# Performance work log

Measured on AMD Instinct MI355X. Metric: run time of the kernel, lower is better.

## Reference

```python
import jax, jax.numpy as jnp
import numpy as np
import math


def _conv1x1(x, w, b):
    # x: [B,C,H,W], w: [O,C], b: [O] -> [B,O,H,W]
    return jnp.einsum('oc,bchw->bohw', w, x) + b[None, :, None, None]


def _attn_branch(x, f_w, f_b, g_w, g_b, h_w, h_b, gamma):
    B, C, H, W = x.shape
    N = H * W
    k_dim = C // 8
    f = _conv1x1(x, f_w, f_b).reshape(B, k_dim, N)  # [B,k,N]
    g = _conv1x1(x, g_w, g_b).reshape(B, k_dim, N)  # [B,k,N]
    # attention[b, n, m] = sum_k f[b,k,n] * g[b,k,m] / sqrt(k_dim)
    scores = jnp.einsum('bkn,bkm->bnm', f, g) / math.sqrt(k_dim)
    attn = jax.nn.softmax(scores, axis=2)  # softmax over last dim (dim=2)
    h = _conv1x1(x, h_w, h_b).reshape(B, C, N)  # [B,C,N]
    sa_map = jnp.einsum('bcn,bnm->bcm', h, attn).reshape(B, C, H, W)
    return gamma[0] * sa_map + x


def setup_inputs() -> dict:
    key = jax.random.key(0)
    ks = jax.random.split(key, 8)
    B, C, H, W = 4, 256, 64, 64
    kd = C // 8
    scale_in = 1.0 / math.sqrt(C)
    return {
        'x1': jax.random.normal(ks[0], (B, C, H, W), jnp.float32),
        'x2': jax.random.normal(ks[1], (B, C, H, W), jnp.float32),
        'f_w': jax.random.normal(ks[2], (kd, C), jnp.float32) * scale_in,
        'f_b': jnp.zeros((kd,), jnp.float32),
        'g_w': jax.random.normal(ks[3], (kd, C), jnp.float32) * scale_in,
        'g_b': jnp.zeros((kd,), jnp.float32),
        'h1_w': jax.random.normal(ks[4], (C, C), jnp.float32) * scale_in,
        'h1_b': jnp.zeros((C,), jnp.float32),
        'h2_w': jax.random.normal(ks[5], (C, C), jnp.float32) * scale_in,
        'h2_b': jnp.zeros((C,), jnp.float32),
        'gamma1': jax.random.normal(ks[6], (1,), jnp.float32),
        'gamma2': jax.random.normal(ks[7], (1,), jnp.float32),
    }


def reference(x1, x2, f_w, f_b, g_w, g_b, h1_w, h1_b, h2_w, h2_b, gamma1, gamma2):
    y1 = _attn_branch(x1, f_w, f_b, g_w, g_b, h1_w, h1_b, gamma1)
    y2 = _attn_branch(x2, f_w, f_b, g_w, g_b, h2_w, h2_b, gamma2)
    return (y1, y2)
```

## Files before the change

### kernel.cpp

```cpp
#include <hip/hip_runtime.h>
#include <hip/hip_bf16.h>
#include <math.h>

#define NDIM 4096
#define CDIM 256
#define KD   32
#define SCALE 0.17677669529663687f
#define SHIFT 8.0f

typedef __attribute__((ext_vector_type(8))) short short8;
typedef __attribute__((ext_vector_type(4))) float f32x4;
typedef unsigned short u16;
typedef unsigned int u32;

__device__ __forceinline__ u32 f2bf(float x) {
  union { float f; u32 u; } v; v.f = x;
  return (v.u + 0x7FFFu + ((v.u >> 16) & 1u)) >> 16;
}

__device__ __forceinline__ u32 pack_bf16x2(float a, float b) {
  __hip_bfloat162 h2 = __float22bfloat162_rn(make_float2(a, b));
  u32 r;
  __builtin_memcpy(&r, &h2, 4);
  return r;
}

#define MFMA16(a, b, c) __builtin_amdgcn_mfma_f32_16x16x32_bf16((a), (b), (c), 0, 0, 0)

__global__ void cast_all_kernel(const float* __restrict__ h1w,
                                const float* __restrict__ h2w,
                                const float* __restrict__ fw,
                                const float* __restrict__ gw,
                                u16* __restrict__ dst) {
  int i = blockIdx.x * 256 + threadIdx.x;
  float v;
  if (i < 65536) v = h1w[i];
  else if (i < 131072) v = h2w[i - 65536];
  else if (i < 139264) v = fw[i - 131072];
  else v = gw[i - 139264];
  dst[i] = (u16)f2bf(v);
}

__global__ __launch_bounds__(256) void transpose_cast_kernel(
    const float* __restrict__ x1, const float* __restrict__ x2,
    u16* __restrict__ xt) {
  __shared__ float ts[64][68];
  const int t = threadIdx.x;
  const int ntile = blockIdx.x * 64, Ctile = blockIdx.y * 64, z = blockIdx.z;
  const float* xb = ((z >> 2) ? x2 : x1) + (size_t)(z & 3) * CDIM * NDIM;
  u16* xtb = xt + (size_t)z * NDIM * CDIM;
  const int r = t >> 4, c4 = (t & 15) * 4;
#pragma unroll
  for (int i = 0; i < 4; i++) {
    float4 v = *(const float4*)&xb[(size_t)(Ctile + r + i * 16) * NDIM + ntile + c4];
    *(float4*)&ts[r + i * 16][c4] = v;
  }
  __syncthreads();
  const int n = t >> 2, Cg = (t & 3) * 16;
  u32 pk[8];
#pragma unroll
  for (int j = 0; j < 8; j++) {
    u32 lo = f2bf(ts[Cg + 2 * j][n]);
    u32 hi = f2bf(ts[Cg + 2 * j + 1][n]);
    pk[j] = lo | (hi << 16);
  }
  uint4* dst = (uint4*)&xtb[(size_t)(ntile + n) * CDIM + Ctile + Cg];
  dst[0] = make_uint4(pk[0], pk[1], pk[2], pk[3]);
  dst[1] = make_uint4(pk[4], pk[5], pk[6], pk[7]);
}

__global__ __launch_bounds__(256) void conv_fg_kernel(
    const u16* __restrict__ Wf, const float* __restrict__ fbias,
    const u16* __restrict__ Wg, const float* __restrict__ gbias,
    const u16* __restrict__ xt, u16* __restrict__ ftT, u16* __restrict__ gtT) {
  const int t = threadIdx.x, w = t >> 6, l = t & 63, li = l & 15, q = l >> 4;
  const int ntile = blockIdx.x * 64, bb = blockIdx.y;
  const u16* xtb = xt + (size_t)bb * NDIM * CDIM;
  f32x4 zero4 = {0.f, 0.f, 0.f, 0.f};
  f32x4 acc[2][2];
  for (int i = 0; i < 2; i++) for (int j = 0; j < 2; j++) acc[i][j] = zero4;
  const int nrow = ntile + w * 16 + li;

  for (int k0 = 0; k0 < CDIM; k0 += 32) {
    short8 bx = *(const short8*)&xtb[(size_t)nrow * CDIM + k0 + q * 8];
    short8 af0 = *(const short8*)&Wf[(size_t)(li) * CDIM + k0 + q * 8];
    short8 af1 = *(const short8*)&Wf[(size_t)(16 + li) * CDIM + k0 + q * 8];
    short8 ag0 = *(const short8*)&Wg[(size_t)(li) * CDIM + k0 + q * 8];
    short8 ag1 = *(const short8*)&Wg[(size_t)(16 + li) * CDIM + k0 + q * 8];
    acc[0][0] = MFMA16(af0, bx, acc[0][0]);
    acc[0][1] = MFMA16(af1, bx, acc[0][1]);
    acc[1][0] = MFMA16(ag0, bx, acc[1][0]);
    acc[1][1] = MFMA16(ag1, bx, acc[1][1]);
  }
  u16* outs[2] = {ftT + (size_t)bb * NDIM * KD, gtT + (size_t)bb * NDIM * KD};
  const float* biases[2] = {fbias, gbias};
#pragma unroll
  for (int fg = 0; fg < 2; fg++) {
#pragma unroll
    for (int os = 0; os < 2; os++) {
      float b0 = biases[fg][os * 16 + q * 4 + 0];
      float b1 = biases[fg][os * 16 + q * 4 + 1];
      float b2 = biases[fg][os * 16 + q * 4 + 2];
      float b3 = biases[fg][os * 16 + q * 4 + 3];
      u32 p0 = f2bf(acc[fg][os][0] + b0) | (f2bf(acc[fg][os][1] + b1) << 16);
      u32 p1 = f2bf(acc[fg][os][2] + b2) | (f2bf(acc[fg][os][3] + b3) << 16);
      *(uint2*)&outs[fg][(size_t)nrow * KD + os * 16 + q * 4] = make_uint2(p0, p1);
    }
  }
}

__global__ __launch_bounds__(256) void stats_kernel(
    const u16* __restrict__ ft, const u16* __restrict__ gt,
    float* __restrict__ L) {
  __shared__ float zred[32][64];
  const int t = threadIdx.x, w = t >> 6, l = t & 63, li = l & 15, q = l >> 4;
  const int n0 = blockIdx.x * 32;
  const int bb = blockIdx.z * 4 + blockIdx.y;
  const u16* ftb = ft + (size_t)bb * NDIM * KD;
  const u16* gtb = gt + (size_t)bb * NDIM * KD;
  f32x4 zero4 = {0.f, 0.f, 0.f, 0.f};

  short8 a0 = *(const short8*)&ftb[(size_t)(n0 + li) * KD + q * 8];
  short8 a1 = *(const short8*)&ftb[(size_t)(n0 + 16 + li) * KD + q * 8];
  f32x4 z0 = zero4, z1 = zero4;

#pragma unroll 2
  for (int it = 0; it < 64; it++) {
    int m = (it * 4 + w) * 16;
    short8 bf = *(const short8*)&gtb[(size_t)(m + li) * KD + q * 8];
    f32x4 S0 = MFMA16(a0, bf, zero4);
    f32x4 S1 = MFMA16(a1, bf, zero4);
#pragma unroll
    for (int reg = 0; reg < 4; reg++) {
      z0[reg] += __expf(S0[reg] * SCALE - SHIFT);
      z1[reg] += __expf(S1[reg] * SCALE - SHIFT);
    }
  }
#pragma unroll
  for (int reg = 0; reg < 4; reg++) {
    zred[q * 4 + reg][w * 16 + li] = z0[reg];
    zred[16 + q * 4 + reg][w * 16 + li] = z1[reg];
  }
  __syncthreads();
  const int r = t >> 3, i8 = t & 7;
  float4 s1 = *(const float4*)&zred[r][i8 * 8];
  float4 s2 = *(const float4*)&zred[r][i8 * 8 + 4];
  float sum = s1.x + s1.y + s1.z + s1.w + s2.x + s2.y + s2.z + s2.w;
  sum += __shfl_xor(sum, 1, 8);
  sum += __shfl_xor(sum, 2, 8);
  sum += __shfl_xor(sum, 4, 8);
  if (i8 == 0) L[(size_t)bb * NDIM + n0 + r] = SHIFT + __logf(sum);
}

__global__ __launch_bounds__(256) void conv_h_kernel(
    const u16* __restrict__ Wall, const float* __restrict__ b1,
    const float* __restrict__ b2, const u16* __restrict__ xt,
    const float* __restrict__ L, u16* __restrict__ outH) {
  const int t = threadIdx.x, w = t >> 6, l = t & 63, li = l & 15, q = l >> 4;
  const int ntile = blockIdx.x * 64;
  const int o0 = blockIdx.y * 64 + w * 16;
  const int bb = blockIdx.z, branch = bb >> 2;
  const u16* W = Wall + (size_t)branch * CDIM * CDIM;
  const float* bias = branch ? b2 : b1;
  const u16* xtb = xt + (size_t)bb * NDIM * CDIM;
  const float* Lb = L + (size_t)bb * NDIM;
  u16* ob = outH + (size_t)bb * CDIM * NDIM;
  f32x4 zero4 = {0.f, 0.f, 0.f, 0.f};
  f32x4 acc[4];
  for (int i = 0; i < 4; i++) acc[i] = zero4;

  for (int k0 = 0; k0 < CDIM; k0 += 32) {
    short8 a = *(const short8*)&W[(size_t)(o0 + li) * CDIM + k0 + q * 8];
#pragma unroll
    for (int ns = 0; ns < 4; ns++) {
      short8 bf = *(const short8*)&xtb[(size_t)(ntile + ns * 16 + li) * CDIM + k0 + q * 8];
      acc[ns] = MFMA16(a, bf, acc[ns]);
    }
  }
  float bv[4];
#pragma unroll
  for (int reg = 0; reg < 4; reg++) bv[reg] = bias[o0 + q * 4 + reg];
#pragma unroll
  for (int ns = 0; ns < 4; ns++) {
    int n = ntile + ns * 16 + li;
    float ex = __expf(-Lb[n]);
#pragma unroll
    for (int reg = 0; reg < 4; reg++) {
      int c = o0 + q * 4 + reg;
      ob[(size_t)c * NDIM + n] = (u16)f2bf((acc[ns][reg] + bv[reg]) * ex);
    }
  }
}

__global__ __launch_bounds__(1024, 4) void apply_kernel(
    const u16* __restrict__ ft, const u16* __restrict__ gt,
    const u16* __restrict__ h,
    const float* __restrict__ x1, const float* __restrict__ x2,
    const float* __restrict__ gamma1, const float* __restrict__ gamma2,
    float* __restrict__ out) {
  __shared__ u16 Pt[2][128][132];
  const int t = threadIdx.x, w = t >> 6, l = t & 63, li = l & 15, q = l >> 4;
  const int bid = blockIdx.x;
  const int bb = bid & 7;
  const int mtile = (bid >> 3) * 128;
  const int br = bb >> 2, b = bb & 3;
  const u16* ftb = ft + (size_t)bb * NDIM * KD;
  const u16* gtb = gt + (size_t)bb * NDIM * KD;
  const u16* hb = h + (size_t)bb * CDIM * NDIM;
  const float* xb = (br ? x2 : x1) + (size_t)b * CDIM * NDIM;
  const float gmv = br ? gamma2[0] : gamma1[0];
  float* ob = out + (size_t)bb * CDIM * NDIM;

  const bool producer = (w & 1) == 0;
  const int pidx = w >> 1;
  const int c0 = (w >> 1) * 32;
  f32x4 zero4 = {0.f, 0.f, 0.f, 0.f};

  short8 gfrag;
  if (producer)
    gfrag = *(const short8*)&gtb[(size_t)(mtile + pidx * 16 + li) * KD + q * 8];

  f32x4 acc[8][2];
#pragma unroll
  for (int i = 0; i < 8; i++)
#pragma unroll
    for (int j = 0; j < 2; j++) acc[i][j] = zero4;

  for (int i = 0; i <= 32; i++) {
    if (producer) {
      if (i < 32) {
        const int n0 = i * 128, buf = i & 1;
        short8 af[8];
#pragma unroll
        for (int j = 0; j < 8; j++)
          af[j] = *(const short8*)&ftb[(size_t)(n0 + j * 16 + li) * KD + q * 8];
#pragma unroll
        for (int j = 0; j < 8; j++) {
          f32x4 S = MFMA16(af[j], gfrag, zero4);
          u32 p0 = pack_bf16x2(__expf(S[0] * SCALE), __expf(S[1] * SCALE));
          u32 p1 = pack_bf16x2(__expf(S[2] * SCALE), __expf(S[3] * SCALE));
          *(uint2*)&Pt[buf][pidx * 16 + li][j * 16 + q * 4] = make_uint2(p0, p1);
        }
      }
    } else {
      if (i >= 1) {
        const int n0 = (i - 1) * 128, buf = (i - 1) & 1;
        short8 ah[2][2];
#pragma unroll
        for (int cs = 0; cs < 2; cs++)
          ah[0][cs] = *(const short8*)
              &hb[(size_t)(c0 + cs * 16 + li) * NDIM + n0 + q * 8];
        __builtin_amdgcn_s_setprio(1);
#pragma unroll
        for (int kh = 0; kh < 4; kh++) {
          if (kh < 3) {
#pragma unroll
            for (int cs = 0; cs < 2; cs++)
              ah[(kh + 1) & 1][cs] = *(const short8*)
                  &hb[(size_t)(c0 + cs * 16 + li) * NDIM + n0 + (kh + 1) * 32 + q * 8];
          }
#pragma unroll
          for (int ms = 0; ms < 8; ms++) {
            short8 bm = *(const short8*)&Pt[buf][ms * 16 + li][kh * 32 + q * 8];
            acc[ms][0] = MFMA16(bm, ah[kh & 1][0], acc[ms][0]);
            acc[ms][1] = MFMA16(bm, ah[kh & 1][1], acc[ms][1]);
          }
        }
        __builtin_amdgcn_s_setprio(0);
      }
    }
    asm volatile("s_waitcnt lgkmcnt(0)" ::: "memory");
    __builtin_amdgcn_s_barrier();
  }

  if (!producer) {
#pragma unroll
    for (int ms = 0; ms < 8; ms++) {
#pragma unroll
      for (int cs = 0; cs < 2; cs++) {
        int c = c0 + cs * 16 + li;
        int m = mtile + ms * 16 + q * 4;
        size_t idx = (size_t)c * NDIM + m;
        float4 xv = *(const float4*)&xb[idx];
        float4 o;
        o.x = gmv * acc[ms][cs][0] + xv.x;
        o.y = gmv * acc[ms][cs][1] + xv.y;
        o.z = gmv * acc[ms][cs][2] + xv.z;
        o.w = gmv * acc[ms][cs][3] + xv.w;
        *(float4*)&ob[idx] = o;
      }
    }
  }
}

extern "C" void kernel_launch(void* const* d_in, const int* in_sizes, int n_in,
                              void* d_out, int out_size, void* d_ws, size_t ws_size,
                              hipStream_t stream) {
  const float* x1 = (const float*)d_in[0];
  const float* x2 = (const float*)d_in[1];
  const float* f_w = (const float*)d_in[2];
  const float* f_b = (const float*)d_in[3];
  const float* g_w = (const float*)d_in[4];
  const float* g_b = (const float*)d_in[5];
  const float* h1_w = (const float*)d_in[6];
  const float* h1_b = (const float*)d_in[7];
  const float* h2_w = (const float*)d_in[8];
  const float* h2_b = (const float*)d_in[9];
  const float* gamma1 = (const float*)d_in[10];
  const float* gamma2 = (const float*)d_in[11];
  float* out = (float*)d_out;

  char* ws = (char*)d_ws;
  u16* xt  = (u16*)(ws);
  u16* wh  = (u16*)(ws + 16777216);
  u16* ftw = (u16*)(ws + 33554432);
  u16* gtw = (u16*)(ws + 35651584);
  u16* wWh = (u16*)(ws + 37748736);
  u16* wWf = (u16*)(ws + 38010880);
  u16* wWg = (u16*)(ws + 38027264);
  float* Lw = (float*)(ws + 38043648);

  cast_all_kernel<<<576, 256, 0, stream>>>(h1_w, h2_w, f_w, g_w, wWh);

  transpose_cast_kernel<<<dim3(64, 4, 8), 256, 0, stream>>>(x1, x2, xt);

  conv_fg_kernel<<<dim3(64, 8), 256, 0, stream>>>(wWf, f_b, wWg, g_b, xt, ftw, gtw);

  stats_kernel<<<dim3(128, 4, 2), 256, 0, stream>>>(ftw, gtw, Lw);

  conv_h_kernel<<<dim3(64, 4, 8), 256, 0, stream>>>(wWh, h1_b, h2_b, xt, Lw, wh);

  apply_kernel<<<256, 1024, 0, stream>>>(ftw, gtw, wh, x1, x2,
                                         gamma1, gamma2, out);
}
```

Measured before the change: 306.9 us.

## Switch apply consumer to 32x32x16 MFMA tiles and fold softmax scale into f weights

The consumer waves in the apply kernel now compute 64x64 output tiles using 32x32x16 bf16 MFMA instead of 16x16x32. Each h and P fragment is reused across two MFMAs, and the per-k-step register double-buffering of h loads is dropped. Separately, the score scale times log2(e) is folded into the bf16 f weights and bias, so the exponentials become plain exp2 without a multiply, and the stats and conv kernels switch to base-2 log and exp. The epilogue now writes scalar floats, which adds uncoalesced-width stores, and folding the scale into bf16 weights changes rounding slightly.

```diff
diff --git a/kernel.cpp b/kernel.cpp
--- a/kernel.cpp
+++ b/kernel.cpp
@@ -6,10 +6,12 @@
 #define CDIM 256
 #define KD   32
 #define SCALE 0.17677669529663687f
-#define SHIFT 8.0f
+#define ALPHA (0.17677669529663687f * 1.44269504088896341f)
+#define SHIFT2 11.541560327111707f
 
 typedef __attribute__((ext_vector_type(8))) short short8;
 typedef __attribute__((ext_vector_type(4))) float f32x4;
+typedef __attribute__((ext_vector_type(16))) float f32x16;
 typedef unsigned short u16;
 typedef unsigned int u32;
 
@@ -26,6 +28,7 @@
 }
 
 #define MFMA16(a, b, c) __builtin_amdgcn_mfma_f32_16x16x32_bf16((a), (b), (c), 0, 0, 0)
+#define MFMA32(a, b, c) __builtin_amdgcn_mfma_f32_32x32x16_bf16((a), (b), (c), 0, 0, 0)
 
 __global__ void cast_all_kernel(const float* __restrict__ h1w,
                                 const float* __restrict__ h2w,
@@ -36,7 +39,7 @@
   float v;
   if (i < 65536) v = h1w[i];
   else if (i < 131072) v = h2w[i - 65536];
-  else if (i < 139264) v = fw[i - 131072];
+  else if (i < 139264) v = fw[i - 131072] * ALPHA;
   else v = gw[i - 139264];
   dst[i] = (u16)f2bf(v);
 }
@@ -94,14 +97,15 @@
   }
   u16* outs[2] = {ftT + (size_t)bb * NDIM * KD, gtT + (size_t)bb * NDIM * KD};
   const float* biases[2] = {fbias, gbias};
+  const float bscale[2] = {ALPHA, 1.0f};
 #pragma unroll
   for (int fg = 0; fg < 2; fg++) {
 #pragma unroll
     for (int os = 0; os < 2; os++) {
-      float b0 = biases[fg][os * 16 + q * 4 + 0];
-      float b1 = biases[fg][os * 16 + q * 4 + 1];
-      float b2 = biases[fg][os * 16 + q * 4 + 2];
-      float b3 = biases[fg][os * 16 + q * 4 + 3];
+      float b0 = biases[fg][os * 16 + q * 4 + 0] * bscale[fg];
+      float b1 = biases[fg][os * 16 + q * 4 + 1] * bscale[fg];
+      float b2 = biases[fg][os * 16 + q * 4 + 2] * bscale[fg];
+      float b3 = biases[fg][os * 16 + q * 4 + 3] * bscale[fg];
       u32 p0 = f2bf(acc[fg][os][0] + b0) | (f2bf(acc[fg][os][1] + b1) << 16);
       u32 p1 = f2bf(acc[fg][os][2] + b2) | (f2bf(acc[fg][os][3] + b3) << 16);
       *(uint2*)&outs[fg][(size_t)nrow * KD + os * 16 + q * 4] = make_uint2(p0, p1);
@@ -132,8 +136,8 @@
     f32x4 S1 = MFMA16(a1, bf, zero4);
 #pragma unroll
     for (int reg = 0; reg < 4; reg++) {
-      z0[reg] += __expf(S0[reg] * SCALE - SHIFT);
-      z1[reg] += __expf(S1[reg] * SCALE - SHIFT);
+      z0[reg] += exp2f(S0[reg] - SHIFT2);
+      z1[reg] += exp2f(S1[reg] - SHIFT2);
     }
   }
 #pragma unroll
@@ -149,7 +153,7 @@
   sum += __shfl_xor(sum, 1, 8);
   sum += __shfl_xor(sum, 2, 8);
   sum += __shfl_xor(sum, 4, 8);
-  if (i8 == 0) L[(size_t)bb * NDIM + n0 + r] = SHIFT + __logf(sum);
+  if (i8 == 0) L[(size_t)bb * NDIM + n0 + r] = SHIFT2 + __log2f(sum);
 }
 
 __global__ __launch_bounds__(256) void conv_h_kernel(
@@ -183,7 +187,7 @@
 #pragma unroll
   for (int ns = 0; ns < 4; ns++) {
     int n = ntile + ns * 16 + li;
-    float ex = __expf(-Lb[n]);
+    float ex = exp2f(-Lb[n]);
 #pragma unroll
     for (int reg = 0; reg < 4; reg++) {
       int c = o0 + q * 4 + reg;
@@ -213,18 +217,23 @@
 
   const bool producer = (w & 1) == 0;
   const int pidx = w >> 1;
-  const int c0 = (w >> 1) * 32;
+  const int cidx = w >> 1;
+  const int mbase = (cidx >> 2) * 64;
+  const int c0 = (cidx & 3) * 64;
+  const int l31 = l & 31, lh = l >> 5;
   f32x4 zero4 = {0.f, 0.f, 0.f, 0.f};
 
   short8 gfrag;
   if (producer)
     gfrag = *(const short8*)&gtb[(size_t)(mtile + pidx * 16 + li) * KD + q * 8];
 
-  f32x4 acc[8][2];
-#pragma unroll
-  for (int i = 0; i < 8; i++)
-#pragma unroll
-    for (int j = 0; j < 2; j++) acc[i][j] = zero4;
+  f32x16 acc[2][2];
+#pragma unroll
+  for (int i = 0; i < 2; i++)
+#pragma unroll
+    for (int j = 0; j < 2; j++)
+#pragma unroll
+      for (int r = 0; r < 16; r++) acc[i][j][r] = 0.f;
 
   for (int i = 0; i <= 32; i++) {
     if (producer) {
@@ -237,34 +246,27 @@
 #pragma unroll
         for (int j = 0; j < 8; j++) {
           f32x4 S = MFMA16(af[j], gfrag, zero4);
-          u32 p0 = pack_bf16x2(__expf(S[0] * SCALE), __expf(S[1] * SCALE));
-          u32 p1 = pack_bf16x2(__expf(S[2] * SCALE), __expf(S[3] * SCALE));
+          u32 p0 = pack_bf16x2(exp2f(S[0]), exp2f(S[1]));
+          u32 p1 = pack_bf16x2(exp2f(S[2]), exp2f(S[3]));
           *(uint2*)&Pt[buf][pidx * 16 + li][j * 16 + q * 4] = make_uint2(p0, p1);
         }
       }
     } else {
       if (i >= 1) {
         const int n0 = (i - 1) * 128, buf = (i - 1) & 1;
-        short8 ah[2][2];
-#pragma unroll
-        for (int cs = 0; cs < 2; cs++)
-          ah[0][cs] = *(const short8*)
-              &hb[(size_t)(c0 + cs * 16 + li) * NDIM + n0 + q * 8];
         __builtin_amdgcn_s_setprio(1);
 #pragma unroll
-        for (int kh = 0; kh < 4; kh++) {
-          if (kh < 3) {
-#pragma unroll
-            for (int cs = 0; cs < 2; cs++)
-              ah[(kh + 1) & 1][cs] = *(const short8*)
-                  &hb[(size_t)(c0 + cs * 16 + li) * NDIM + n0 + (kh + 1) * 32 + q * 8];
-          }
-#pragma unroll
-          for (int ms = 0; ms < 8; ms++) {
-            short8 bm = *(const short8*)&Pt[buf][ms * 16 + li][kh * 32 + q * 8];
-            acc[ms][0] = MFMA16(bm, ah[kh & 1][0], acc[ms][0]);
-            acc[ms][1] = MFMA16(bm, ah[kh & 1][1], acc[ms][1]);
-          }
+        for (int ks = 0; ks < 8; ks++) {
+          short8 ah0 = *(const short8*)
+              &hb[(size_t)(c0 + l31) * NDIM + n0 + ks * 16 + lh * 8];
+          short8 ah1 = *(const short8*)
+              &hb[(size_t)(c0 + 32 + l31) * NDIM + n0 + ks * 16 + lh * 8];
+          short8 bm0 = *(const short8*)&Pt[buf][mbase + l31][ks * 16 + lh * 8];
+          short8 bm1 = *(const short8*)&Pt[buf][mbase + 32 + l31][ks * 16 + lh * 8];
+          acc[0][0] = MFMA32(ah0, bm0, acc[0][0]);
+          acc[0][1] = MFMA32(ah1, bm0, acc[0][1]);
+          acc[1][0] = MFMA32(ah0, bm1, acc[1][0]);
+          acc[1][1] = MFMA32(ah1, bm1, acc[1][1]);
         }
         __builtin_amdgcn_s_setprio(0);
       }
@@ -275,19 +277,16 @@
 
   if (!producer) {
 #pragma unroll
-    for (int ms = 0; ms < 8; ms++) {
-#pragma unroll
-      for (int cs = 0; cs < 2; cs++) {
-        int c = c0 + cs * 16 + li;
-        int m = mtile + ms * 16 + q * 4;
-        size_t idx = (size_t)c * NDIM + m;
-        float4 xv = *(const float4*)&xb[idx];
-        float4 o;
-        o.x = gmv * acc[ms][cs][0] + xv.x;
-        o.y = gmv * acc[ms][cs][1] + xv.y;
-        o.z = gmv * acc[ms][cs][2] + xv.z;
-        o.w = gmv * acc[ms][cs][3] + xv.w;
-        *(float4*)&ob[idx] = o;
+    for (int mt = 0; mt < 2; mt++) {
+#pragma unroll
+      for (int ct = 0; ct < 2; ct++) {
+#pragma unroll
+        for (int reg = 0; reg < 16; reg++) {
+          int c = c0 + ct * 32 + (reg & 3) + 8 * (reg >> 2) + 4 * lh;
+          int m = mtile + mbase + mt * 32 + l31;
+          size_t idx = (size_t)c * NDIM + m;
+          ob[idx] = gmv * acc[mt][ct][reg] + xb[idx];
+        }
       }
     }
   }
```

Measured after the change: 372.5 us. 21.4% more time.

## Fold softmax scale into f weights, use exp2, retile apply consumer warps

Applied to the files above, without the earlier changes.

Folds the 1/sqrt(k)·log2(e) factor into the f projection weights and bias, so the score exponentials become plain exp2 calls with no per-element multiply. Consumer warps in the apply kernel switch from 128m×32c tiles to 64m×64c tiles, which halves LDS reads of the P tile per MFMA while doubling the h fragments loaded per warp. The LDS row pitch is also changed from 132 to 136 elements to alter bank mapping. Rounding f to bf16 after scaling slightly changes precision.

```diff
diff --git a/kernel.cpp b/kernel.cpp
--- a/kernel.cpp
+++ b/kernel.cpp
@@ -6,7 +6,8 @@
 #define CDIM 256
 #define KD   32
 #define SCALE 0.17677669529663687f
-#define SHIFT 8.0f
+#define ALPHA (0.17677669529663687f * 1.44269504088896341f)
+#define SHIFT2 11.541560327111707f
 
 typedef __attribute__((ext_vector_type(8))) short short8;
 typedef __attribute__((ext_vector_type(4))) float f32x4;
@@ -36,7 +37,7 @@
   float v;
   if (i < 65536) v = h1w[i];
   else if (i < 131072) v = h2w[i - 65536];
-  else if (i < 139264) v = fw[i - 131072];
+  else if (i < 139264) v = fw[i - 131072] * ALPHA;
   else v = gw[i - 139264];
   dst[i] = (u16)f2bf(v);
 }
@@ -94,14 +95,15 @@
   }
   u16* outs[2] = {ftT + (size_t)bb * NDIM * KD, gtT + (size_t)bb * NDIM * KD};
   const float* biases[2] = {fbias, gbias};
+  const float bscale[2] = {ALPHA, 1.0f};
 #pragma unroll
   for (int fg = 0; fg < 2; fg++) {
 #pragma unroll
     for (int os = 0; os < 2; os++) {
-      float b0 = biases[fg][os * 16 + q * 4 + 0];
-      float b1 = biases[fg][os * 16 + q * 4 + 1];
-      float b2 = biases[fg][os * 16 + q * 4 + 2];
-      float b3 = biases[fg][os * 16 + q * 4 + 3];
+      float b0 = biases[fg][os * 16 + q * 4 + 0] * bscale[fg];
+      float b1 = biases[fg][os * 16 + q * 4 + 1] * bscale[fg];
+      float b2 = biases[fg][os * 16 + q * 4 + 2] * bscale[fg];
+      float b3 = biases[fg][os * 16 + q * 4 + 3] * bscale[fg];
       u32 p0 = f2bf(acc[fg][os][0] + b0) | (f2bf(acc[fg][os][1] + b1) << 16);
       u32 p1 = f2bf(acc[fg][os][2] + b2) | (f2bf(acc[fg][os][3] + b3) << 16);
       *(uint2*)&outs[fg][(size_t)nrow * KD + os * 16 + q * 4] = make_uint2(p0, p1);
@@ -132,8 +134,8 @@
     f32x4 S1 = MFMA16(a1, bf, zero4);
 #pragma unroll
     for (int reg = 0; reg < 4; reg++) {
-      z0[reg] += __expf(S0[reg] * SCALE - SHIFT);
-      z1[reg] += __expf(S1[reg] * SCALE - SHIFT);
+      z0[reg] += exp2f(S0[reg] - SHIFT2);
+      z1[reg] += exp2f(S1[reg] - SHIFT2);
     }
   }
 #pragma unroll
@@ -149,7 +151,7 @@
   sum += __shfl_xor(sum, 1, 8);
   sum += __shfl_xor(sum, 2, 8);
   sum += __shfl_xor(sum, 4, 8);
-  if (i8 == 0) L[(size_t)bb * NDIM + n0 + r] = SHIFT + __logf(sum);
+  if (i8 == 0) L[(size_t)bb * NDIM + n0 + r] = SHIFT2 + __log2f(sum);
 }
 
 __global__ __launch_bounds__(256) void conv_h_kernel(
@@ -183,7 +185,7 @@
 #pragma unroll
   for (int ns = 0; ns < 4; ns++) {
     int n = ntile + ns * 16 + li;
-    float ex = __expf(-Lb[n]);
+    float ex = exp2f(-Lb[n]);
 #pragma unroll
     for (int reg = 0; reg < 4; reg++) {
       int c = o0 + q * 4 + reg;
@@ -198,7 +200,7 @@
     const float* __restrict__ x1, const float* __restrict__ x2,
     const float* __restrict__ gamma1, const float* __restrict__ gamma2,
     float* __restrict__ out) {
-  __shared__ u16 Pt[2][128][132];
+  __shared__ u16 Pt[2][128][136];
   const int t = threadIdx.x, w = t >> 6, l = t & 63, li = l & 15, q = l >> 4;
   const int bid = blockIdx.x;
   const int bb = bid & 7;
@@ -213,18 +215,20 @@
 
   const bool producer = (w & 1) == 0;
   const int pidx = w >> 1;
-  const int c0 = (w >> 1) * 32;
+  const int cidx = w >> 1;
+  const int mbase = (cidx >> 2) * 64;
+  const int c0 = (cidx & 3) * 64;
   f32x4 zero4 = {0.f, 0.f, 0.f, 0.f};
 
   short8 gfrag;
   if (producer)
     gfrag = *(const short8*)&gtb[(size_t)(mtile + pidx * 16 + li) * KD + q * 8];
 
-  f32x4 acc[8][2];
-#pragma unroll
-  for (int i = 0; i < 8; i++)
-#pragma unroll
-    for (int j = 0; j < 2; j++) acc[i][j] = zero4;
+  f32x4 acc[4][4];
+#pragma unroll
+  for (int i = 0; i < 4; i++)
+#pragma unroll
+    for (int j = 0; j < 4; j++) acc[i][j] = zero4;
 
   for (int i = 0; i <= 32; i++) {
     if (producer) {
@@ -237,17 +241,17 @@
 #pragma unroll
         for (int j = 0; j < 8; j++) {
           f32x4 S = MFMA16(af[j], gfrag, zero4);
-          u32 p0 = pack_bf16x2(__expf(S[0] * SCALE), __expf(S[1] * SCALE));
-          u32 p1 = pack_bf16x2(__expf(S[2] * SCALE), __expf(S[3] * SCALE));
+          u32 p0 = pack_bf16x2(exp2f(S[0]), exp2f(S[1]));
+          u32 p1 = pack_bf16x2(exp2f(S[2]), exp2f(S[3]));
           *(uint2*)&Pt[buf][pidx * 16 + li][j * 16 + q * 4] = make_uint2(p0, p1);
         }
       }
     } else {
       if (i >= 1) {
         const int n0 = (i - 1) * 128, buf = (i - 1) & 1;
-        short8 ah[2][2];
-#pragma unroll
-        for (int cs = 0; cs < 2; cs++)
+        short8 ah[2][4];
+#pragma unroll
+        for (int cs = 0; cs < 4; cs++)
           ah[0][cs] = *(const short8*)
               &hb[(size_t)(c0 + cs * 16 + li) * NDIM + n0 + q * 8];
         __builtin_amdgcn_s_setprio(1);
@@ -255,15 +259,17 @@
         for (int kh = 0; kh < 4; kh++) {
           if (kh < 3) {
 #pragma unroll
-            for (int cs = 0; cs < 2; cs++)
+            for (int cs = 0; cs < 4; cs++)
               ah[(kh + 1) & 1][cs] = *(const short8*)
                   &hb[(size_t)(c0 + cs * 16 + li) * NDIM + n0 + (kh + 1) * 32 + q * 8];
           }
 #pragma unroll
-          for (int ms = 0; ms < 8; ms++) {
-            short8 bm = *(const short8*)&Pt[buf][ms * 16 + li][kh * 32 + q * 8];
+          for (int ms = 0; ms < 4; ms++) {
+            short8 bm = *(const short8*)&Pt[buf][mbase + ms * 16 + li][kh * 32 + q * 8];
             acc[ms][0] = MFMA16(bm, ah[kh & 1][0], acc[ms][0]);
             acc[ms][1] = MFMA16(bm, ah[kh & 1][1], acc[ms][1]);
+            acc[ms][2] = MFMA16(bm, ah[kh & 1][2], acc[ms][2]);
+            acc[ms][3] = MFMA16(bm, ah[kh & 1][3], acc[ms][3]);
           }
         }
         __builtin_amdgcn_s_setprio(0);
@@ -275,11 +281,11 @@
 
   if (!producer) {
 #pragma unroll
-    for (int ms = 0; ms < 8; ms++) {
-#pragma unroll
-      for (int cs = 0; cs < 2; cs++) {
+    for (int ms = 0; ms < 4; ms++) {
+#pragma unroll
+      for (int cs = 0; cs < 4; cs++) {
         int c = c0 + cs * 16 + li;
-        int m = mtile + ms * 16 + q * 4;
+        int m = mtile + mbase + ms * 16 + q * 4;
         size_t idx = (size_t)c * NDIM + m;
         float4 xv = *(const float4*)&xb[idx];
         float4 o;
```

New measurement: 382.9 us. +24.8%, slower.
